# Kernel optimization log

Hardware: AMD Instinct MI355X
Metric: run time of the kernel (lower is better)

Reference implementation:

```python
import jax, jax.numpy as jnp
import numpy as np

L, H, C, HS, E, K, V, BS = 2, 12, 768, 64, 8, 2, 32000, 1024
B, T = 2, 1024


def layer_norm(x, s, b):
    mu = x.mean(-1, keepdims=True)
    var = ((x - mu) ** 2).mean(-1, keepdims=True)
    return (x - mu) / jnp.sqrt(var + 1e-5) * s + b


def setup_inputs() -> dict:
    key = jax.random.key(0)
    ks = jax.random.split(key, 16)
    def n(k, shape, s=0.02):
        return jax.random.normal(k, shape, dtype=jnp.float32) * s
    return {
        'idx': jax.random.randint(ks[0], (B, T), 0, V),
        'targets': jax.random.randint(ks[1], (B, T), 0, V),
        'tok_emb': n(ks[2], (V, C)),
        'pos_emb': n(ks[3], (BS, C)),
        'ln1_s': jnp.ones((L, C), jnp.float32), 'ln1_b': jnp.zeros((L, C), jnp.float32),
        'wq': n(ks[4], (L, H, C, HS)), 'wk': n(ks[5], (L, H, C, HS)), 'wv': n(ks[6], (L, H, C, HS)),
        'wo': n(ks[7], (L, C, C)), 'bo': jnp.zeros((L, C), jnp.float32),
        'ln2_s': jnp.ones((L, C), jnp.float32), 'ln2_b': jnp.zeros((L, C), jnp.float32),
        'gate_w': n(ks[8], (L, E, C)),
        'w1': n(ks[9], (L, E, 4 * C, C)), 'b1': jnp.zeros((L, E, 4 * C), jnp.float32),
        'w2': n(ks[10], (L, E, C, 4 * C)), 'b2': jnp.zeros((L, E, C), jnp.float32),
        'lm_w': n(ks[11], (V, C)), 'lm_b': jnp.zeros((V,), jnp.float32),
    }


def reference(idx, targets, tok_emb, pos_emb, ln1_s, ln1_b, wq, wk, wv, wo, bo,
              ln2_s, ln2_b, gate_w, w1, b1, w2, b2, lm_w, lm_b):
    Bsz, Tn = idx.shape
    x = tok_emb[idx] + pos_emb[:Tn]                       # [B,T,C]
    mask = jnp.tril(jnp.ones((Tn, Tn), bool))
    for l in range(L):
        # causal multi-head attention (per-head projections, scale = n_embed**-0.5 as in source)
        h = layer_norm(x, ln1_s[l], ln1_b[l])
        q = jnp.einsum('btc,hcd->bhtd', h, wq[l])
        k = jnp.einsum('btc,hcd->bhtd', h, wk[l])
        v = jnp.einsum('btc,hcd->bhtd', h, wv[l])
        att = jnp.einsum('bhtd,bhsd->bhts', q, k) * (C ** -0.5)
        att = jax.nn.softmax(jnp.where(mask, att, -jnp.inf), axis=-1)
        o = jnp.einsum('bhts,bhsd->bhtd', att, v)
        o = o.transpose(0, 2, 1, 3).reshape(Bsz, Tn, C)   # concat heads
        x = x + jnp.einsum('btc,oc->bto', o, wo[l]) + bo[l]
        # MoE FFN: top-k routing, softmax over selected gate logits
        h2 = layer_norm(x, ln2_s[l], ln2_b[l]).reshape(-1, C)     # [N,C]
        gl = jnp.einsum('tc,ec->te', h2, gate_w[l])               # [N,E]
        wts, sel = jax.lax.top_k(gl, K)
        wts = jax.nn.softmax(wts, axis=-1)
        comb = jnp.einsum('tk,tke->te', wts, jax.nn.one_hot(sel, E, dtype=wts.dtype))
        hid = jax.nn.relu(jnp.einsum('tc,efc->etf', h2, w1[l]) + b1[l][:, None, :])
        y = jnp.einsum('etf,ecf->etc', hid, w2[l]) + b2[l][:, None, :]
        moe = jnp.einsum('te,etc->tc', comb, y)                   # dispatch-weighted combine
        x = x + moe.reshape(Bsz, Tn, C)
    logits = jnp.einsum('btc,vc->btv', x, lm_w) + lm_b
    lf = logits.reshape(-1, V)
    tf = targets.reshape(-1)
    loss = -jnp.take_along_axis(jax.nn.log_softmax(lf, axis=-1), tf[:, None], axis=1).mean()
    return lf, loss
```

## Files before the change

### kernel.cpp

```cpp
#include <hip/hip_runtime.h>
#include <hip/hip_bf16.h>

#define LCNT 2
#define HCNT 12
#define CDIM 768
#define HSD  64
#define ECNT 8
#define VOC  32000
#define BB   2
#define TT   1024
#define NTOK 2048
#define FF   3072
#define QKVLD 2304
#define TOTCAP 5120

typedef __attribute__((ext_vector_type(8))) short bf16x8;
typedef __attribute__((ext_vector_type(4))) float f32x4;

__device__ __forceinline__ float wave_sum(float v) {
    #pragma unroll
    for (int off = 32; off; off >>= 1) v += __shfl_xor(v, off);
    return v;
}
__device__ __forceinline__ float wave_max(float v) {
    #pragma unroll
    for (int off = 32; off; off >>= 1) v = fmaxf(v, __shfl_xor(v, off));
    return v;
}
__device__ __forceinline__ unsigned short f2bf(float f) {
    unsigned int u = __float_as_uint(f);
    unsigned int r = (u + 0x7FFFu + ((u >> 16) & 1u)) >> 16;
    return (unsigned short)r;
}
__device__ __forceinline__ float bf2f(unsigned short h) {
    return __uint_as_float((unsigned int)h << 16);
}
__device__ __forceinline__ void split2(float a, unsigned short& h, unsigned short& l) {
    h = f2bf(a);
    l = f2bf(a - bf2f(h));
}
__device__ __forceinline__ ushort4 cvt4(float4 v) {
    ushort4 r;
    r.x = f2bf(v.x); r.y = f2bf(v.y); r.z = f2bf(v.z); r.w = f2bf(v.w);
    return r;
}

__global__ __launch_bounds__(256)
void cvt_bf16_kernel(const float* __restrict__ in, unsigned short* __restrict__ out, int n4)
{
    for (int i = blockIdx.x * 256 + threadIdx.x; i < n4; i += gridDim.x * 256) {
        float4 v = reinterpret_cast<const float4*>(in)[i];
        reinterpret_cast<ushort4*>(out)[i] = cvt4(v);
    }
}

__global__ __launch_bounds__(256)
void embed_kernel(const int* __restrict__ idx, const float* __restrict__ tok,
                  const float* __restrict__ pos, float* __restrict__ x)
{
    int i = blockIdx.x * 256 + threadIdx.x;
    int c = i % CDIM;
    int n = i / CDIM;
    int t = n % TT;
    x[i] = tok[(size_t)idx[n] * CDIM + c] + pos[(size_t)t * CDIM + c];
}

__global__ __launch_bounds__(256)
void repack_kernel(const float* __restrict__ wq, const float* __restrict__ wk,
                   const float* __restrict__ wv, float* __restrict__ wp)
{
    int i = blockIdx.x * 256 + threadIdx.x;
    int kk = i % CDIM;
    int n  = (i / CDIM) % CDIM;
    int w3 = (i / (CDIM * CDIM)) % 3;
    int l  = i / (CDIM * CDIM * 3);
    const float* src = (w3 == 0) ? wq : (w3 == 1) ? wk : wv;
    int h = n / HSD, d = n % HSD;
    wp[(((size_t)l * 3 + w3) * CDIM + n) * CDIM + kk] =
        src[((((size_t)l * HCNT + h) * CDIM) + kk) * HSD + d];
}

__global__ __launch_bounds__(256)
void ln_kernel(const float* __restrict__ x, const float* __restrict__ sc,
               const float* __restrict__ bs, float* __restrict__ out)
{
    int row = blockIdx.x;
    const float* xr = x + (size_t)row * CDIM;
    float* orow = out + (size_t)row * CDIM;
    int tid = threadIdx.x;
    float v0 = xr[tid], v1 = xr[tid + 256], v2 = xr[tid + 512];
    float s1 = v0 + v1 + v2;
    float s2 = v0 * v0 + v1 * v1 + v2 * v2;
    s1 = wave_sum(s1);
    s2 = wave_sum(s2);
    __shared__ float r1[4], r2[4];
    int w = tid >> 6, lane = tid & 63;
    if (lane == 0) { r1[w] = s1; r2[w] = s2; }
    __syncthreads();
    float t1 = r1[0] + r1[1] + r1[2] + r1[3];
    float t2 = r2[0] + r2[1] + r2[2] + r2[3];
    float mu = t1 * (1.0f / CDIM);
    float var = t2 * (1.0f / CDIM) - mu * mu;
    float rstd = rsqrtf(var + 1e-5f);
    orow[tid]       = (v0 - mu) * rstd * sc[tid]       + bs[tid];
    orow[tid + 256] = (v1 - mu) * rstd * sc[tid + 256] + bs[tid + 256];
    orow[tid + 512] = (v2 - mu) * rstd * sc[tid + 512] + bs[tid + 512];
}

#define BM 128
#define BN 128
#define BK 32
#define PADK 40

template<int MODE, bool SPLIT>
__global__ __launch_bounds__(256)
void gemm_bf16_kernel(int Kd,
                      const float* __restrict__ A, int lda,
                      const float* __restrict__ B, int ldb,
                      const float* __restrict__ bias,
                      float* __restrict__ out, int ldo,
                      const int* __restrict__ rowmeta,
                      size_t bstride, int biasstride)
{
    __shared__ short Ah[BM * PADK];
    __shared__ short Bh[BN * PADK];
    __shared__ short Al[SPLIT ? BM * PADK : 2];
    __shared__ short Bl[SPLIT ? BN * PADK : 2];

    int roff = 0;
    if (rowmeta) {
        const int ee = blockIdx.z;
        const int rcnt = rowmeta[2 * ee + 1];
        if ((int)(blockIdx.y * BM) >= rcnt) return;
        roff = rowmeta[2 * ee];
        B += (size_t)ee * bstride;
        if (bias) bias += (size_t)ee * biasstride;
    }

    const int tid = threadIdx.x;
    const int m0 = roff + blockIdx.y * BM;
    const int n0 = blockIdx.x * BN;
    const int w = tid >> 6, lane = tid & 63;
    const int wr = w >> 1, wc = w & 1;
    const int lrow = lane & 15, lkg = lane >> 4;
    const int srow = tid >> 3, skg = (tid & 7) * 4;

    const float* Ablk = A + (size_t)m0 * lda;
    const float* Bblk = B + (size_t)n0 * ldb;

    float4 pa[4], pb[4];
    #pragma unroll
    for (int p = 0; p < 4; ++p) {
        pa[p] = *(const float4*)(Ablk + (size_t)(p * 32 + srow) * lda + skg);
        pb[p] = *(const float4*)(Bblk + (size_t)(p * 32 + srow) * ldb + skg);
    }

    f32x4 acc[4][4] = {};
    const int nk = Kd / BK;

    for (int t = 0; t < nk; ++t) {
        __syncthreads();
        #pragma unroll
        for (int p = 0; p < 4; ++p) {
            if constexpr (SPLIT) {
                ushort4 h, l;
                split2(pa[p].x, h.x, l.x); split2(pa[p].y, h.y, l.y);
                split2(pa[p].z, h.z, l.z); split2(pa[p].w, h.w, l.w);
                *(ushort4*)(&Ah[(p * 32 + srow) * PADK + skg]) = h;
                *(ushort4*)(&Al[(p * 32 + srow) * PADK + skg]) = l;
                split2(pb[p].x, h.x, l.x); split2(pb[p].y, h.y, l.y);
                split2(pb[p].z, h.z, l.z); split2(pb[p].w, h.w, l.w);
                *(ushort4*)(&Bh[(p * 32 + srow) * PADK + skg]) = h;
                *(ushort4*)(&Bl[(p * 32 + srow) * PADK + skg]) = l;
            } else {
                *(ushort4*)(&Ah[(p * 32 + srow) * PADK + skg]) = cvt4(pa[p]);
                *(ushort4*)(&Bh[(p * 32 + srow) * PADK + skg]) = cvt4(pb[p]);
            }
        }
        __syncthreads();
        if (t + 1 < nk) {
            const int kb = (t + 1) * BK + skg;
            #pragma unroll
            for (int p = 0; p < 4; ++p) {
                pa[p] = *(const float4*)(Ablk + (size_t)(p * 32 + srow) * lda + kb);
                pb[p] = *(const float4*)(Bblk + (size_t)(p * 32 + srow) * ldb + kb);
            }
        }
        bf16x8 afh[4], afl[4];
        #pragma unroll
        for (int i = 0; i < 4; ++i) {
            afh[i] = *(const bf16x8*)(&Ah[(wr * 64 + i * 16 + lrow) * PADK + lkg * 8]);
            if constexpr (SPLIT)
                afl[i] = *(const bf16x8*)(&Al[(wr * 64 + i * 16 + lrow) * PADK + lkg * 8]);
        }
        #pragma unroll
        for (int j = 0; j < 4; ++j) {
            const bf16x8 bh = *(const bf16x8*)(&Bh[(wc * 64 + j * 16 + lrow) * PADK + lkg * 8]);
            if constexpr (SPLIT) {
                const bf16x8 bl = *(const bf16x8*)(&Bl[(wc * 64 + j * 16 + lrow) * PADK + lkg * 8]);
                #pragma unroll
                for (int i = 0; i < 4; ++i) {
                    acc[i][j] = __builtin_amdgcn_mfma_f32_16x16x32_bf16(afh[i], bh, acc[i][j], 0, 0, 0);
                    acc[i][j] = __builtin_amdgcn_mfma_f32_16x16x32_bf16(afl[i], bh, acc[i][j], 0, 0, 0);
                    acc[i][j] = __builtin_amdgcn_mfma_f32_16x16x32_bf16(afh[i], bl, acc[i][j], 0, 0, 0);
                }
            } else {
                #pragma unroll
                for (int i = 0; i < 4; ++i)
                    acc[i][j] = __builtin_amdgcn_mfma_f32_16x16x32_bf16(afh[i], bh, acc[i][j], 0, 0, 0);
            }
        }
    }

    #pragma unroll
    for (int i = 0; i < 4; ++i) {
        #pragma unroll
        for (int r = 0; r < 4; ++r) {
            const int row = m0 + wr * 64 + i * 16 + lkg * 4 + r;
            #pragma unroll
            for (int j = 0; j < 4; ++j) {
                const int col = n0 + wc * 64 + j * 16 + lrow;
                const float bj = bias ? bias[col] : 0.0f;
                const float vres = acc[i][j][r] + bj;
                float* op = out + (size_t)row * ldo + col;
                if (MODE == 0) *op = vres;
                else if (MODE == 1) *op = *op + vres;
                else *op = fmaxf(vres, 0.0f);
            }
        }
    }
}

template<int MODE, bool SWZ, bool OUTBF, bool BBF>
__global__ __launch_bounds__(256)
void gemm_fastw_kernel(int Kd,
                       const unsigned short* __restrict__ A, int lda,
                       const void* __restrict__ Bv, int ldb,
                       const float* __restrict__ bias,
                       void* __restrict__ outv, int ldo,
                       const int* __restrict__ rowmeta,
                       size_t bstride, int biasstride)
{
    __shared__ short Ah[BM * PADK];
    __shared__ short Bh[BN * PADK];

    int bx = blockIdx.x, by = blockIdx.y;
    if constexpr (SWZ) {
        const int nwg = gridDim.x * gridDim.y;
        const int chunk = nwg >> 3;
        const int flat = by * gridDim.x + bx;
        const int newid = (flat & 7) * chunk + (flat >> 3);
        by = newid % gridDim.y;
        bx = newid / gridDim.y;
    }

    const float* Bf = (const float*)Bv;
    const unsigned short* Bb = (const unsigned short*)Bv;
    float* outf = (float*)outv;
    unsigned short* outb = (unsigned short*)outv;

    int roff = 0;
    if (rowmeta) {
        const int ee = blockIdx.z;
        const int rcnt = rowmeta[2 * ee + 1];
        if ((int)(by * BM) >= rcnt) return;
        roff = rowmeta[2 * ee];
        if (BBF) Bb += (size_t)ee * bstride; else Bf += (size_t)ee * bstride;
        if (bias) bias += (size_t)ee * biasstride;
    }

    const int tid = threadIdx.x;
    const int m0 = roff + by * BM;
    const int n0 = bx * BN;
    const int w = tid >> 6, lane = tid & 63;
    const int wr = w >> 1, wc = w & 1;
    const int lrow = lane & 15, lkg = lane >> 4;
    const int srow = tid >> 3, skg = (tid & 7) * 4;

    const unsigned short* Ablk = A + (size_t)m0 * lda;
    const float* Bfblk = Bf + (size_t)n0 * ldb;
    const unsigned short* Bbblk = Bb + (size_t)n0 * ldb;

    ushort4 pa[4];
    ushort4 pbb[4];
    float4  pbf[4];
    #pragma unroll
    for (int p = 0; p < 4; ++p) {
        pa[p] = *(const ushort4*)(Ablk + (size_t)(p * 32 + srow) * lda + skg);
        if constexpr (BBF) pbb[p] = *(const ushort4*)(Bbblk + (size_t)(p * 32 + srow) * ldb + skg);
        else               pbf[p] = *(const float4*)(Bfblk + (size_t)(p * 32 + srow) * ldb + skg);
    }

    f32x4 acc[4][4] = {};
    const int nk = Kd / BK;

    for (int t = 0; t < nk; ++t) {
        __syncthreads();
        #pragma unroll
        for (int p = 0; p < 4; ++p) {
            *(ushort4*)(&Ah[(p * 32 + srow) * PADK + skg]) = pa[p];
            *(ushort4*)(&Bh[(p * 32 + srow) * PADK + skg]) = BBF ? pbb[p] : cvt4(pbf[p]);
        }
        __syncthreads();
        if (t + 1 < nk) {
            const int kb = (t + 1) * BK + skg;
            #pragma unroll
            for (int p = 0; p < 4; ++p) {
                pa[p] = *(const ushort4*)(Ablk + (size_t)(p * 32 + srow) * lda + kb);
                if constexpr (BBF) pbb[p] = *(const ushort4*)(Bbblk + (size_t)(p * 32 + srow) * ldb + kb);
                else               pbf[p] = *(const float4*)(Bfblk + (size_t)(p * 32 + srow) * ldb + kb);
            }
        }
        bf16x8 af[4];
        #pragma unroll
        for (int i = 0; i < 4; ++i)
            af[i] = *(const bf16x8*)(&Ah[(wr * 64 + i * 16 + lrow) * PADK + lkg * 8]);
        #pragma unroll
        for (int j = 0; j < 4; ++j) {
            const bf16x8 bh = *(const bf16x8*)(&Bh[(wc * 64 + j * 16 + lrow) * PADK + lkg * 8]);
            #pragma unroll
            for (int i = 0; i < 4; ++i)
                acc[i][j] = __builtin_amdgcn_mfma_f32_16x16x32_bf16(af[i], bh, acc[i][j], 0, 0, 0);
        }
    }

    #pragma unroll
    for (int i = 0; i < 4; ++i) {
        #pragma unroll
        for (int r = 0; r < 4; ++r) {
            const int row = m0 + wr * 64 + i * 16 + lkg * 4 + r;
            #pragma unroll
            for (int j = 0; j < 4; ++j) {
                const int col = n0 + wc * 64 + j * 16 + lrow;
                const float bj = bias ? bias[col] : 0.0f;
                float vres = acc[i][j][r] + bj;
                if (MODE == 2) vres = fmaxf(vres, 0.0f);
                if constexpr (OUTBF) outb[(size_t)row * ldo + col] = f2bf(vres);
                else                 outf[(size_t)row * ldo + col] = vres;
            }
        }
    }
}

#define QBLK 64
#define KVBLK 64

__global__ __launch_bounds__(256)
void attn_mfma_kernel(const float* __restrict__ qkv, float* __restrict__ o)
{
    __shared__ short Kh[2][KVBLK][PADK];
    __shared__ short Kl[2][KVBLK][PADK];
    __shared__ short Vh[2][HSD][PADK];
    __shared__ short Vl[2][HSD][PADK];
    __shared__ short Ph[4][2][16][PADK];
    __shared__ short Pl[4][2][16][PADK];

    const int t0 = blockIdx.x * QBLK;
    const int bh = blockIdx.y;
    const int b = bh / HCNT, hh = bh % HCNT;
    const size_t baseq = (size_t)b * TT * QKVLD + (size_t)hh * HSD;
    const size_t obase = (size_t)b * TT * CDIM + (size_t)hh * HSD;
    const float* q = qkv + baseq;
    const float* k = qkv + baseq + CDIM;
    const float* v = qkv + baseq + 2 * CDIM;
    const int tid = threadIdx.x;
    const int w = tid >> 6, lane = tid & 63;
    const int lrow = lane & 15, lkg = lane >> 4;
    const float sscale = rsqrtf((float)CDIM);

    bf16x8 qh[2], ql[2];
    {
        const float* qr = q + (size_t)(t0 + w * 16 + lrow) * QKVLD;
        #pragma unroll
        for (int ks = 0; ks < 2; ++ks) {
            #pragma unroll
            for (int j = 0; j < 8; ++j) {
                unsigned short h, l;
                split2(qr[ks * 32 + lkg * 8 + j], h, l);
                qh[ks][j] = (short)h;
                ql[ks][j] = (short)l;
            }
        }
    }

    f32x4 oacc[4] = {};
    float m_[4], l_[4];
    #pragma unroll
    for (int rr = 0; rr < 4; ++rr) { m_[rr] = -1e30f; l_[rr] = 0.0f; }

    for (int s0 = 0; s0 <= t0 + QBLK - 1; s0 += KVBLK) {
        __syncthreads();
        {
            const int srow = tid >> 3, skg = (tid & 7) * 4;
            #pragma unroll
            for (int p = 0; p < 2; ++p) {
                const float* krow = k + (size_t)(s0 + p * 32 + srow) * QKVLD;
                #pragma unroll
                for (int ks = 0; ks < 2; ++ks) {
                    float4 a = *(const float4*)(krow + ks * 32 + skg);
                    ushort4 h, l;
                    split2(a.x, h.x, l.x); split2(a.y, h.y, l.y);
                    split2(a.z, h.z, l.z); split2(a.w, h.w, l.w);
                    *(ushort4*)(&Kh[ks][p * 32 + srow][skg]) = h;
                    *(ushort4*)(&Kl[ks][p * 32 + srow][skg]) = l;
                }
            }
            const int key = tid & 63, dg = (tid >> 6) * 16;
            const float* vrow = v + (size_t)(s0 + key) * QKVLD + dg;
            const int kst = key >> 5, ko = key & 31;
            #pragma unroll
            for (int dd = 0; dd < 16; dd += 4) {
                float4 a = *(const float4*)(vrow + dd);
                unsigned short h, l;
                split2(a.x, h, l); Vh[kst][dg + dd + 0][ko] = h; Vl[kst][dg + dd + 0][ko] = l;
                split2(a.y, h, l); Vh[kst][dg + dd + 1][ko] = h; Vl[kst][dg + dd + 1][ko] = l;
                split2(a.z, h, l); Vh[kst][dg + dd + 2][ko] = h; Vl[kst][dg + dd + 2][ko] = l;
                split2(a.w, h, l); Vh[kst][dg + dd + 3][ko] = h; Vl[kst][dg + dd + 3][ko] = l;
            }
        }
        __syncthreads();

        f32x4 sacc[4] = {};
        #pragma unroll
        for (int j = 0; j < 4; ++j) {
            #pragma unroll
            for (int ks = 0; ks < 2; ++ks) {
                const bf16x8 bh = *(const bf16x8*)(&Kh[ks][j * 16 + lrow][lkg * 8]);
                const bf16x8 bl = *(const bf16x8*)(&Kl[ks][j * 16 + lrow][lkg * 8]);
                sacc[j] = __builtin_amdgcn_mfma_f32_16x16x32_bf16(qh[ks], bh, sacc[j], 0, 0, 0);
                sacc[j] = __builtin_amdgcn_mfma_f32_16x16x32_bf16(ql[ks], bh, sacc[j], 0, 0, 0);
                sacc[j] = __builtin_amdgcn_mfma_f32_16x16x32_bf16(qh[ks], bl, sacc[j], 0, 0, 0);
            }
        }

        #pragma unroll
        for (int rr = 0; rr < 4; ++rr) {
            const int qi = t0 + w * 16 + lkg * 4 + rr;
            float pv[4];
            float mx = -1e30f;
            #pragma unroll
            for (int j = 0; j < 4; ++j) {
                float s = sacc[j][rr] * sscale;
                if (s0 + j * 16 + lrow > qi) s = -1e30f;
                pv[j] = s;
                mx = fmaxf(mx, s);
            }
            #pragma unroll
            for (int off = 1; off < 16; off <<= 1) mx = fmaxf(mx, __shfl_xor(mx, off));
            const float mnew = fmaxf(m_[rr], mx);
            const float corr = __expf(m_[rr] - mnew);
            float ps = 0.0f;
            #pragma unroll
            for (int j = 0; j < 4; ++j) { pv[j] = __expf(pv[j] - mnew); ps += pv[j]; }
            #pragma unroll
            for (int off = 1; off < 16; off <<= 1) ps += __shfl_xor(ps, off);
            l_[rr] = l_[rr] * corr + ps;
            m_[rr] = mnew;
            #pragma unroll
            for (int jd = 0; jd < 4; ++jd) oacc[jd][rr] *= corr;
            #pragma unroll
            for (int j = 0; j < 4; ++j) {
                unsigned short h, l;
                split2(pv[j], h, l);
                const int key = j * 16 + lrow;
                Ph[w][key >> 5][lkg * 4 + rr][key & 31] = h;
                Pl[w][key >> 5][lkg * 4 + rr][key & 31] = l;
            }
        }

        #pragma unroll
        for (int ks = 0; ks < 2; ++ks) {
            const bf16x8 ah = *(const bf16x8*)(&Ph[w][ks][lrow][lkg * 8]);
            const bf16x8 al = *(const bf16x8*)(&Pl[w][ks][lrow][lkg * 8]);
            #pragma unroll
            for (int jd = 0; jd < 4; ++jd) {
                const bf16x8 bh = *(const bf16x8*)(&Vh[ks][jd * 16 + lrow][lkg * 8]);
                const bf16x8 bl = *(const bf16x8*)(&Vl[ks][jd * 16 + lrow][lkg * 8]);
                oacc[jd] = __builtin_amdgcn_mfma_f32_16x16x32_bf16(ah, bh, oacc[jd], 0, 0, 0);
                oacc[jd] = __builtin_amdgcn_mfma_f32_16x16x32_bf16(al, bh, oacc[jd], 0, 0, 0);
                oacc[jd] = __builtin_amdgcn_mfma_f32_16x16x32_bf16(ah, bl, oacc[jd], 0, 0, 0);
            }
        }
    }

    #pragma unroll
    for (int rr = 0; rr < 4; ++rr) {
        const int qi = t0 + w * 16 + lkg * 4 + rr;
        const float invl = 1.0f / l_[rr];
        float* orow = o + obase + (size_t)qi * CDIM;
        #pragma unroll
        for (int jd = 0; jd < 4; ++jd)
            orow[jd * 16 + lrow] = oacc[jd][rr] * invl;
    }
}

__global__ __launch_bounds__(256)
void gate_kernel(const float* __restrict__ h2, const float* __restrict__ gw,
                 int2* __restrict__ sel, float2* __restrict__ wts)
{
    __shared__ float gws[ECNT * CDIM];
    int tid = threadIdx.x;
    for (int i = tid; i < ECNT * CDIM; i += 256) gws[i] = gw[i];
    __syncthreads();
    int t = blockIdx.x * 256 + tid;
    const float* hr = h2 + (size_t)t * CDIM;
    float g[ECNT] = {};
    for (int c = 0; c < CDIM; ++c) {
        float hv = hr[c];
        #pragma unroll
        for (int e = 0; e < ECNT; ++e) g[e] = fmaf(hv, gws[e * CDIM + c], g[e]);
    }
    int e0 = 0; float g0 = g[0];
    #pragma unroll
    for (int e = 1; e < ECNT; ++e) if (g[e] > g0) { g0 = g[e]; e0 = e; }
    int e1 = -1; float g1 = -1e30f;
    #pragma unroll
    for (int e = 0; e < ECNT; ++e) if (e != e0 && g[e] > g1) { g1 = g[e]; e1 = e; }
    float z = __expf(g1 - g0);
    float w0 = 1.0f / (1.0f + z);
    sel[t] = make_int2(e0, e1);
    wts[t] = make_float2(w0, 1.0f - w0);
}

__global__ __launch_bounds__(256)
void route_kernel(const int2* __restrict__ sel, int* __restrict__ perm,
                  int* __restrict__ tokpos, int* __restrict__ meta)
{
    __shared__ int cnt[ECNT], off[ECNT], cur[ECNT];
    const int tid = threadIdx.x;
    if (tid < ECNT) cnt[tid] = 0;
    __syncthreads();
    for (int t = tid; t < NTOK; t += 256) {
        atomicAdd(&cnt[sel[t].x], 1);
        atomicAdd(&cnt[sel[t].y], 1);
    }
    __syncthreads();
    if (tid == 0) {
        int run = 0;
        for (int e = 0; e < ECNT; ++e) {
            off[e] = run; cur[e] = 0;
            int pc = (cnt[e] + BM - 1) / BM * BM;
            meta[2 * e] = run; meta[2 * e + 1] = pc;
            run += pc;
        }
    }
    __syncthreads();
    for (int p = tid; p < TOTCAP; p += 256) perm[p] = 0;
    __syncthreads();
    for (int t = tid; t < NTOK; t += 256) {
        int2 s = sel[t];
        int p0 = atomicAdd(&cur[s.x], 1); perm[off[s.x] + p0] = t; tokpos[2 * t]     = off[s.x] + p0;
        int p1 = atomicAdd(&cur[s.y], 1); perm[off[s.y] + p1] = t; tokpos[2 * t + 1] = off[s.y] + p1;
    }
}

__global__ __launch_bounds__(256)
void gather_kernel(const float* __restrict__ h2, const int* __restrict__ perm,
                   float* __restrict__ xg)
{
    int i = blockIdx.x * 256 + threadIdx.x;
    int c = i % CDIM, p = i / CDIM;
    xg[i] = h2[(size_t)perm[p] * CDIM + c];
}

__global__ __launch_bounds__(256)
void gather_bf16_kernel(const float* __restrict__ h2, const int* __restrict__ perm,
                        unsigned short* __restrict__ xg)
{
    int i = blockIdx.x * 256 + threadIdx.x;
    int c = i % CDIM, p = i / CDIM;
    xg[i] = f2bf(h2[(size_t)perm[p] * CDIM + c]);
}

__global__ __launch_bounds__(256)
void combine_kernel(const float* __restrict__ y, const int* __restrict__ tokpos,
                    const float2* __restrict__ wts, float* __restrict__ x)
{
    int i = blockIdx.x * 256 + threadIdx.x;
    int c = i % CDIM, t = i / CDIM;
    float2 wv = wts[t];
    x[i] += wv.x * y[(size_t)tokpos[2 * t] * CDIM + c]
          + wv.y * y[(size_t)tokpos[2 * t + 1] * CDIM + c];
}

__global__ __launch_bounds__(256)
void loss_row_kernel(const float* __restrict__ logits, const int* __restrict__ tgt,
                     float* __restrict__ lrow)
{
    int row = blockIdx.x;
    const float* lr = logits + (size_t)row * VOC;
    int tid = threadIdx.x, w = tid >> 6, lane = tid & 63;
    __shared__ float red[4];
    float mx = -1e30f;
    for (int i = tid; i < VOC; i += 256) mx = fmaxf(mx, lr[i]);
    mx = wave_max(mx);
    if (lane == 0) red[w] = mx;
    __syncthreads();
    mx = fmaxf(fmaxf(red[0], red[1]), fmaxf(red[2], red[3]));
    __syncthreads();
    float se = 0.0f;
    for (int i = tid; i < VOC; i += 256) se += expf(lr[i] - mx);
    se = wave_sum(se);
    if (lane == 0) red[w] = se;
    __syncthreads();
    if (tid == 0) {
        float lse = mx + logf(red[0] + red[1] + red[2] + red[3]);
        lrow[row] = lse - lr[tgt[row]];
    }
}

__global__ __launch_bounds__(256)
void loss_reduce_kernel(const float* __restrict__ lrow, float* __restrict__ out)
{
    int tid = threadIdx.x, w = tid >> 6, lane = tid & 63;
    float s = 0.0f;
    for (int i = tid; i < NTOK; i += 256) s += lrow[i];
    s = wave_sum(s);
    __shared__ float red[4];
    if (lane == 0) red[w] = s;
    __syncthreads();
    if (tid == 0) out[0] = (red[0] + red[1] + red[2] + red[3]) * (1.0f / NTOK);
}

extern "C" void kernel_launch(void* const* d_in, const int* in_sizes, int n_in,
                              void* d_out, int out_size, void* d_ws, size_t ws_size,
                              hipStream_t stream)
{
    const int*   idx     = (const int*)d_in[0];
    const int*   targets = (const int*)d_in[1];
    const float* tok_emb = (const float*)d_in[2];
    const float* pos_emb = (const float*)d_in[3];
    const float* ln1_s   = (const float*)d_in[4];
    const float* ln1_b   = (const float*)d_in[5];
    const float* wq      = (const float*)d_in[6];
    const float* wk      = (const float*)d_in[7];
    const float* wv      = (const float*)d_in[8];
    const float* wo      = (const float*)d_in[9];
    const float* bo      = (const float*)d_in[10];
    const float* ln2_s   = (const float*)d_in[11];
    const float* ln2_b   = (const float*)d_in[12];
    const float* gate_w  = (const float*)d_in[13];
    const float* w1      = (const float*)d_in[14];
    const float* b1      = (const float*)d_in[15];
    const float* w2      = (const float*)d_in[16];
    const float* b2      = (const float*)d_in[17];
    const float* lm_w    = (const float*)d_in[18];
    const float* lm_b    = (const float*)d_in[19];
    float* out = (float*)d_out;

    float* ws   = (float*)d_ws;
    float* wp   = ws;
    float* x    = wp   + (size_t)3 * LCNT * CDIM * CDIM;
    float* hbuf = x    + (size_t)NTOK * CDIM;
    float* qkv  = hbuf + (size_t)NTOK * CDIM;
    float* xg   = qkv  + (size_t)NTOK * QKVLD;
    float* hid  = xg   + (size_t)TOTCAP * CDIM;
    float* lrow = hid  + (size_t)TOTCAP * FF;
    float2* wts = (float2*)(lrow + NTOK);
    int2*  sel  = (int2*)(wts + NTOK);
    int*   perm = (int*)(sel + NTOK);
    int*  tokpos= perm + TOTCAP;
    int*   meta = tokpos + 2 * NTOK;
    unsigned short* x_bf = (unsigned short*)(meta + 16);

    unsigned short* xg_bf  = (unsigned short*)xg;
    unsigned short* hid_bf = (unsigned short*)hid;
    unsigned short* lmw_bf = (unsigned short*)hid;

    dim3 blk(256);

    repack_kernel<<<(3 * LCNT * CDIM * CDIM) / 256, blk, 0, stream>>>(wq, wk, wv, wp);
    embed_kernel<<<(NTOK * CDIM) / 256, blk, 0, stream>>>(idx, tok_emb, pos_emb, x);

    for (int l = 0; l < LCNT; ++l) {
        ln_kernel<<<NTOK, blk, 0, stream>>>(x, ln1_s + (size_t)l * CDIM, ln1_b + (size_t)l * CDIM, hbuf);

        gemm_bf16_kernel<0, true><<<dim3(QKVLD / BN, NTOK / BM), blk, 0, stream>>>(
            CDIM, hbuf, CDIM, wp + (size_t)l * 3 * CDIM * CDIM, CDIM,
            nullptr, qkv, QKVLD, nullptr, 0, 0);

        attn_mfma_kernel<<<dim3(TT / QBLK, BB * HCNT), blk, 0, stream>>>(qkv, hbuf);

        gemm_bf16_kernel<1, true><<<dim3(CDIM / BN, NTOK / BM), blk, 0, stream>>>(
            CDIM, hbuf, CDIM, wo + (size_t)l * CDIM * CDIM, CDIM,
            bo + (size_t)l * CDIM, x, CDIM, nullptr, 0, 0);

        float* h2 = qkv;
        float* ybuf = qkv;
        ln_kernel<<<NTOK, blk, 0, stream>>>(x, ln2_s + (size_t)l * CDIM, ln2_b + (size_t)l * CDIM, h2);
        gate_kernel<<<NTOK / 256, blk, 0, stream>>>(h2, gate_w + (size_t)l * ECNT * CDIM, sel, wts);
        route_kernel<<<1, blk, 0, stream>>>(sel, perm, tokpos, meta);

        const float* w1l = w1 + (size_t)l * ECNT * FF * CDIM;
        const float* b1l = b1 + (size_t)l * ECNT * FF;
        const float* w2l = w2 + (size_t)l * ECNT * CDIM * FF;
        const float* b2l = b2 + (size_t)l * ECNT * CDIM;
        if (l == 0) {
            gather_kernel<<<(TOTCAP * CDIM) / 256, blk, 0, stream>>>(h2, perm, xg);
            gemm_bf16_kernel<2, true><<<dim3(FF / BN, TOTCAP / BM, ECNT), blk, 0, stream>>>(
                CDIM, xg, CDIM, w1l, CDIM, b1l, hid, FF, meta, (size_t)FF * CDIM, FF);
            gemm_bf16_kernel<0, true><<<dim3(CDIM / BN, TOTCAP / BM, ECNT), blk, 0, stream>>>(
                FF, hid, FF, w2l, FF, b2l, ybuf, CDIM, meta, (size_t)CDIM * FF, CDIM);
        } else {
            gather_bf16_kernel<<<(TOTCAP * CDIM) / 256, blk, 0, stream>>>(h2, perm, xg_bf);
            gemm_fastw_kernel<2, false, true, false><<<dim3(FF / BN, TOTCAP / BM, ECNT), blk, 0, stream>>>(
                CDIM, xg_bf, CDIM, w1l, CDIM, b1l, hid_bf, FF, meta, (size_t)FF * CDIM, FF);
            gemm_fastw_kernel<0, false, false, false><<<dim3(CDIM / BN, TOTCAP / BM, ECNT), blk, 0, stream>>>(
                FF, hid_bf, FF, w2l, FF, b2l, ybuf, CDIM, meta, (size_t)CDIM * FF, CDIM);
        }
        combine_kernel<<<(NTOK * CDIM) / 256, blk, 0, stream>>>(ybuf, tokpos, wts, x);
    }

    cvt_bf16_kernel<<<2048, blk, 0, stream>>>(lm_w, lmw_bf, VOC * CDIM / 4);
    cvt_bf16_kernel<<<512, blk, 0, stream>>>(x, x_bf, NTOK * CDIM / 4);

    gemm_fastw_kernel<0, true, false, true><<<dim3(VOC / BN, NTOK / BM), blk, 0, stream>>>(
        CDIM, x_bf, CDIM, lmw_bf, CDIM, lm_b, out, VOC, nullptr, 0, 0);

    loss_row_kernel<<<NTOK, blk, 0, stream>>>(out, targets, lrow);
    loss_reduce_kernel<<<1, blk, 0, stream>>>(lrow, out + (size_t)NTOK * VOC);
}
```

Baseline: 1.437 ms.

## Pre-split attention weights to bf16 hi/lo and use direct-to-LDS loads for LM head

QKV and output-projection weights are now pre-split once into bf16 high/low pairs, in the repack step and a new split kernel. A new split-precision GEMM reads them directly instead of re-splitting fp32 weights in every tile. The LM-head GEMM switches to a new kernel that loads bf16 tiles straight into LDS with global_load_lds, skipping the register staging and padded layout. The trade-offs are extra workspace and a one-time split pass. The LDS-direct kernel has no prefetch or double buffering and uses an unpadded layout that may cause bank conflicts.

```diff
diff --git a/kernel.cpp b/kernel.cpp
--- a/kernel.cpp
+++ b/kernel.cpp
@@ -44,6 +44,12 @@
     r.x = f2bf(v.x); r.y = f2bf(v.y); r.z = f2bf(v.z); r.w = f2bf(v.w);
     return r;
 }
+__device__ __forceinline__ void gload16(const void* g, void* l) {
+    __builtin_amdgcn_global_load_lds(
+        (const __attribute__((address_space(1))) unsigned int*)g,
+        (__attribute__((address_space(3))) unsigned int*)l,
+        16, 0, 0);
+}
 
 __global__ __launch_bounds__(256)
 void cvt_bf16_kernel(const float* __restrict__ in, unsigned short* __restrict__ out, int n4)
@@ -51,6 +57,20 @@
     for (int i = blockIdx.x * 256 + threadIdx.x; i < n4; i += gridDim.x * 256) {
         float4 v = reinterpret_cast<const float4*>(in)[i];
         reinterpret_cast<ushort4*>(out)[i] = cvt4(v);
+    }
+}
+
+__global__ __launch_bounds__(256)
+void splitw_kernel(const float* __restrict__ in, unsigned short* __restrict__ oh,
+                   unsigned short* __restrict__ ol, int n4)
+{
+    for (int i = blockIdx.x * 256 + threadIdx.x; i < n4; i += gridDim.x * 256) {
+        float4 v = reinterpret_cast<const float4*>(in)[i];
+        ushort4 h, l;
+        split2(v.x, h.x, l.x); split2(v.y, h.y, l.y);
+        split2(v.z, h.z, l.z); split2(v.w, h.w, l.w);
+        reinterpret_cast<ushort4*>(oh)[i] = h;
+        reinterpret_cast<ushort4*>(ol)[i] = l;
     }
 }
 
@@ -67,7 +87,8 @@
 
 __global__ __launch_bounds__(256)
 void repack_kernel(const float* __restrict__ wq, const float* __restrict__ wk,
-                   const float* __restrict__ wv, float* __restrict__ wp)
+                   const float* __restrict__ wv, unsigned short* __restrict__ wph,
+                   unsigned short* __restrict__ wpl)
 {
     int i = blockIdx.x * 256 + threadIdx.x;
     int kk = i % CDIM;
@@ -76,8 +97,12 @@
     int l  = i / (CDIM * CDIM * 3);
     const float* src = (w3 == 0) ? wq : (w3 == 1) ? wk : wv;
     int h = n / HSD, d = n % HSD;
-    wp[(((size_t)l * 3 + w3) * CDIM + n) * CDIM + kk] =
-        src[((((size_t)l * HCNT + h) * CDIM) + kk) * HSD + d];
+    float v = src[((((size_t)l * HCNT + h) * CDIM) + kk) * HSD + d];
+    unsigned short hh, ll;
+    split2(v, hh, ll);
+    size_t o = (((size_t)l * 3 + w3) * CDIM + n) * CDIM + kk;
+    wph[o] = hh;
+    wpl[o] = ll;
 }
 
 __global__ __launch_bounds__(256)
@@ -231,6 +256,103 @@
     }
 }
 
+template<int MODE>
+__global__ __launch_bounds__(256)
+void gemm_splitpb_kernel(int Kd,
+                         const float* __restrict__ A, int lda,
+                         const unsigned short* __restrict__ Bhg,
+                         const unsigned short* __restrict__ Blg, int ldb,
+                         const float* __restrict__ bias,
+                         float* __restrict__ out, int ldo)
+{
+    __shared__ short Ah[BM * PADK];
+    __shared__ short Al[BM * PADK];
+    __shared__ short Bh[BN * PADK];
+    __shared__ short Bl[BN * PADK];
+
+    const int tid = threadIdx.x;
+    const int m0 = blockIdx.y * BM;
+    const int n0 = blockIdx.x * BN;
+    const int w = tid >> 6, lane = tid & 63;
+    const int wr = w >> 1, wc = w & 1;
+    const int lrow = lane & 15, lkg = lane >> 4;
+    const int srow = tid >> 3, skg = (tid & 7) * 4;
+
+    const float* Ablk = A + (size_t)m0 * lda;
+    const unsigned short* Bhblk = Bhg + (size_t)n0 * ldb;
+    const unsigned short* Blblk = Blg + (size_t)n0 * ldb;
+
+    float4 pa[4];
+    ushort4 pbh[4], pbl[4];
+    #pragma unroll
+    for (int p = 0; p < 4; ++p) {
+        pa[p]  = *(const float4*)(Ablk + (size_t)(p * 32 + srow) * lda + skg);
+        pbh[p] = *(const ushort4*)(Bhblk + (size_t)(p * 32 + srow) * ldb + skg);
+        pbl[p] = *(const ushort4*)(Blblk + (size_t)(p * 32 + srow) * ldb + skg);
+    }
+
+    f32x4 acc[4][4] = {};
+    const int nk = Kd / BK;
+
+    for (int t = 0; t < nk; ++t) {
+        __syncthreads();
+        #pragma unroll
+        for (int p = 0; p < 4; ++p) {
+            ushort4 h, l;
+            split2(pa[p].x, h.x, l.x); split2(pa[p].y, h.y, l.y);
+            split2(pa[p].z, h.z, l.z); split2(pa[p].w, h.w, l.w);
+            *(ushort4*)(&Ah[(p * 32 + srow) * PADK + skg]) = h;
+            *(ushort4*)(&Al[(p * 32 + srow) * PADK + skg]) = l;
+            *(ushort4*)(&Bh[(p * 32 + srow) * PADK + skg]) = pbh[p];
+            *(ushort4*)(&Bl[(p * 32 + srow) * PADK + skg]) = pbl[p];
+        }
+        __syncthreads();
+        if (t + 1 < nk) {
+            const int kb = (t + 1) * BK + skg;
+            #pragma unroll
+            for (int p = 0; p < 4; ++p) {
+                pa[p]  = *(const float4*)(Ablk + (size_t)(p * 32 + srow) * lda + kb);
+                pbh[p] = *(const ushort4*)(Bhblk + (size_t)(p * 32 + srow) * ldb + kb);
+                pbl[p] = *(const ushort4*)(Blblk + (size_t)(p * 32 + srow) * ldb + kb);
+            }
+        }
+        bf16x8 afh[4], afl[4];
+        #pragma unroll
+        for (int i = 0; i < 4; ++i) {
+            afh[i] = *(const bf16x8*)(&Ah[(wr * 64 + i * 16 + lrow) * PADK + lkg * 8]);
+            afl[i] = *(const bf16x8*)(&Al[(wr * 64 + i * 16 + lrow) * PADK + lkg * 8]);
+        }
+        #pragma unroll
+        for (int j = 0; j < 4; ++j) {
+            const bf16x8 bh = *(const bf16x8*)(&Bh[(wc * 64 + j * 16 + lrow) * PADK + lkg * 8]);
+            const bf16x8 bl = *(const bf16x8*)(&Bl[(wc * 64 + j * 16 + lrow) * PADK + lkg * 8]);
+            #pragma unroll
+            for (int i = 0; i < 4; ++i) {
+                acc[i][j] = __builtin_amdgcn_mfma_f32_16x16x32_bf16(afh[i], bh, acc[i][j], 0, 0, 0);
+                acc[i][j] = __builtin_amdgcn_mfma_f32_16x16x32_bf16(afl[i], bh, acc[i][j], 0, 0, 0);
+                acc[i][j] = __builtin_amdgcn_mfma_f32_16x16x32_bf16(afh[i], bl, acc[i][j], 0, 0, 0);
+            }
+        }
+    }
+
+    #pragma unroll
+    for (int i = 0; i < 4; ++i) {
+        #pragma unroll
+        for (int r = 0; r < 4; ++r) {
+            const int row = m0 + wr * 64 + i * 16 + lkg * 4 + r;
+            #pragma unroll
+            for (int j = 0; j < 4; ++j) {
+                const int col = n0 + wc * 64 + j * 16 + lrow;
+                const float bj = bias ? bias[col] : 0.0f;
+                const float vres = acc[i][j][r] + bj;
+                float* op = out + (size_t)row * ldo + col;
+                if (MODE == 0) *op = vres;
+                else *op = *op + vres;
+            }
+        }
+    }
+}
+
 template<int MODE, bool SWZ, bool OUTBF, bool BBF>
 __global__ __launch_bounds__(256)
 void gemm_fastw_kernel(int Kd,
@@ -337,6 +459,80 @@
                 if (MODE == 2) vres = fmaxf(vres, 0.0f);
                 if constexpr (OUTBF) outb[(size_t)row * ldo + col] = f2bf(vres);
                 else                 outf[(size_t)row * ldo + col] = vres;
+            }
+        }
+    }
+}
+
+template<bool SWZ>
+__global__ __launch_bounds__(256)
+void gemm_lds_kernel(int Kd,
+                     const unsigned short* __restrict__ A, int lda,
+                     const unsigned short* __restrict__ B, int ldb,
+                     const float* __restrict__ bias,
+                     float* __restrict__ out, int ldo)
+{
+    __shared__ unsigned short Asl[BM * BK];
+    __shared__ unsigned short Bsl[BN * BK];
+
+    int bx = blockIdx.x, by = blockIdx.y;
+    if constexpr (SWZ) {
+        const int nwg = gridDim.x * gridDim.y;
+        const int chunk = nwg >> 3;
+        const int flat = by * gridDim.x + bx;
+        const int newid = (flat & 7) * chunk + (flat >> 3);
+        by = newid % gridDim.y;
+        bx = newid / gridDim.y;
+    }
+
+    const int tid = threadIdx.x;
+    const int m0 = by * BM;
+    const int n0 = bx * BN;
+    const int w = tid >> 6, lane = tid & 63;
+    const int wr = w >> 1, wc = w & 1;
+    const int lrow = lane & 15, lkg = lane >> 4;
+    const int grow = lane >> 2, gcol = (lane & 3) * 8;
+
+    const unsigned short* Ablk = A + (size_t)m0 * lda;
+    const unsigned short* Bblk = B + (size_t)n0 * ldb;
+
+    f32x4 acc[4][4] = {};
+    const int nk = Kd / BK;
+
+    for (int t = 0; t < nk; ++t) {
+        const int k0 = t * BK;
+        __syncthreads();
+        #pragma unroll
+        for (int j = 0; j < 2; ++j) {
+            const int rbase = w * 32 + j * 16;
+            gload16(Ablk + (size_t)(rbase + grow) * lda + k0 + gcol, Asl + rbase * BK);
+            gload16(Bblk + (size_t)(rbase + grow) * ldb + k0 + gcol, Bsl + rbase * BK);
+        }
+        __syncthreads();
+
+        bf16x8 af[4];
+        #pragma unroll
+        for (int i = 0; i < 4; ++i)
+            af[i] = *(const bf16x8*)(Asl + (wr * 64 + i * 16 + lrow) * BK + lkg * 8);
+        #pragma unroll
+        for (int j = 0; j < 4; ++j) {
+            const bf16x8 bh = *(const bf16x8*)(Bsl + (wc * 64 + j * 16 + lrow) * BK + lkg * 8);
+            #pragma unroll
+            for (int i = 0; i < 4; ++i)
+                acc[i][j] = __builtin_amdgcn_mfma_f32_16x16x32_bf16(af[i], bh, acc[i][j], 0, 0, 0);
+        }
+    }
+
+    #pragma unroll
+    for (int i = 0; i < 4; ++i) {
+        #pragma unroll
+        for (int r = 0; r < 4; ++r) {
+            const int row = m0 + wr * 64 + i * 16 + lkg * 4 + r;
+            #pragma unroll
+            for (int j = 0; j < 4; ++j) {
+                const int col = n0 + wc * 64 + j * 16 + lrow;
+                const float bj = bias ? bias[col] : 0.0f;
+                out[(size_t)row * ldo + col] = acc[i][j][r] + bj;
             }
         }
     }
@@ -648,9 +844,11 @@
     const float* lm_b    = (const float*)d_in[19];
     float* out = (float*)d_out;
 
-    float* ws   = (float*)d_ws;
-    float* wp   = ws;
-    float* x    = wp   + (size_t)3 * LCNT * CDIM * CDIM;
+    unsigned short* wph = (unsigned short*)d_ws;
+    unsigned short* wpl = wph + (size_t)3 * LCNT * CDIM * CDIM;
+    unsigned short* woh = wpl + (size_t)3 * LCNT * CDIM * CDIM;
+    unsigned short* wol = woh + (size_t)LCNT * CDIM * CDIM;
+    float* x    = (float*)(wol + (size_t)LCNT * CDIM * CDIM);
     float* hbuf = x    + (size_t)NTOK * CDIM;
     float* qkv  = hbuf + (size_t)NTOK * CDIM;
     float* xg   = qkv  + (size_t)NTOK * QKVLD;
@@ -669,21 +867,22 @@
 
     dim3 blk(256);
 
-    repack_kernel<<<(3 * LCNT * CDIM * CDIM) / 256, blk, 0, stream>>>(wq, wk, wv, wp);
+    repack_kernel<<<(3 * LCNT * CDIM * CDIM) / 256, blk, 0, stream>>>(wq, wk, wv, wph, wpl);
+    splitw_kernel<<<1024, blk, 0, stream>>>(wo, woh, wol, LCNT * CDIM * CDIM / 4);
     embed_kernel<<<(NTOK * CDIM) / 256, blk, 0, stream>>>(idx, tok_emb, pos_emb, x);
 
     for (int l = 0; l < LCNT; ++l) {
         ln_kernel<<<NTOK, blk, 0, stream>>>(x, ln1_s + (size_t)l * CDIM, ln1_b + (size_t)l * CDIM, hbuf);
 
-        gemm_bf16_kernel<0, true><<<dim3(QKVLD / BN, NTOK / BM), blk, 0, stream>>>(
-            CDIM, hbuf, CDIM, wp + (size_t)l * 3 * CDIM * CDIM, CDIM,
-            nullptr, qkv, QKVLD, nullptr, 0, 0);
+        gemm_splitpb_kernel<0><<<dim3(QKVLD / BN, NTOK / BM), blk, 0, stream>>>(
+            CDIM, hbuf, CDIM, wph + (size_t)l * 3 * CDIM * CDIM, wpl + (size_t)l * 3 * CDIM * CDIM,
+            CDIM, nullptr, qkv, QKVLD);
 
         attn_mfma_kernel<<<dim3(TT / QBLK, BB * HCNT), blk, 0, stream>>>(qkv, hbuf);
 
-        gemm_bf16_kernel<1, true><<<dim3(CDIM / BN, NTOK / BM), blk, 0, stream>>>(
-            CDIM, hbuf, CDIM, wo + (size_t)l * CDIM * CDIM, CDIM,
-            bo + (size_t)l * CDIM, x, CDIM, nullptr, 0, 0);
+        gemm_splitpb_kernel<1><<<dim3(CDIM / BN, NTOK / BM), blk, 0, stream>>>(
+            CDIM, hbuf, CDIM, woh + (size_t)l * CDIM * CDIM, wol + (size_t)l * CDIM * CDIM,
+            CDIM, bo + (size_t)l * CDIM, x, CDIM);
 
         float* h2 = qkv;
         float* ybuf = qkv;
@@ -714,8 +913,8 @@
     cvt_bf16_kernel<<<2048, blk, 0, stream>>>(lm_w, lmw_bf, VOC * CDIM / 4);
     cvt_bf16_kernel<<<512, blk, 0, stream>>>(x, x_bf, NTOK * CDIM / 4);
 
-    gemm_fastw_kernel<0, true, false, true><<<dim3(VOC / BN, NTOK / BM), blk, 0, stream>>>(
-        CDIM, x_bf, CDIM, lmw_bf, CDIM, lm_b, out, VOC, nullptr, 0, 0);
+    gemm_lds_kernel<true><<<dim3(VOC / BN, NTOK / BM), blk, 0, stream>>>(
+        CDIM, x_bf, CDIM, lmw_bf, CDIM, lm_b, out, VOC);
 
     loss_row_kernel<<<NTOK, blk, 0, stream>>>(out, targets, lrow);
     loss_reduce_kernel<<<1, blk, 0, stream>>>(lrow, out + (size_t)NTOK * VOC);
```

After: 1.409 ms. 1.02x faster.
